# Optimization experiments

Measured on AMD Instinct MI355X. Metric: run time of the kernel, lower is better.

The kernel has to match this reference:

```python
import jax, jax.numpy as jnp
import numpy as np

# NOTE: the original source omits the definitions of QSVT, quantum_lcu_block,
# QuantumSumBlock and KANLayer. We reconstruct the standard math these blocks
# implement in quantum-KAN papers/repos:
#   QSVT(x)            -> vector of Chebyshev polynomials T_1..T_D of the
#                         (squashed) input, the polynomial basis QSVT realizes.
#   quantum_lcu_block  -> linear combination of unitaries: weighted sum of the
#                         QSVT vector normalized by the LCU l1 weight norm.
#   QuantumSumBlock    -> learnable interference sum: mean_k sin(alpha_k * v).
#   KANLayer           -> Chebyshev-KAN layer: spline term (Chebyshev basis
#                         contracted with coeffs) + SiLU base branch + bias.
# Everything is fully vectorized over (B, F) instead of the original per-scalar
# Python loops.

B, F, DEG, C, KBASIS = 16384, 512, 8, 10, 8


def _cheb(x, K):
    """Chebyshev features T_1..T_K of x in (-1, 1): shape x.shape + (K,)."""
    t = jnp.arccos(jnp.clip(x, -1.0, 1.0))
    k = jnp.arange(1, K + 1, dtype=x.dtype)
    return jnp.cos(t[..., None] * k)


def setup_inputs() -> dict:
    key = jax.random.key(0)
    ks = jax.random.split(key, 6)
    return {
        "X": jax.random.normal(ks[0], (B, F), dtype=jnp.float32),
        # nn.Parameter(torch.rand(num_features, degree))
        "lcu_weights": jax.random.uniform(ks[1], (F, DEG), dtype=jnp.float32),
        # one QuantumSumBlock(degree) per feature -> (F, DEG) phases
        "sum_alpha": jax.random.normal(ks[2], (F, DEG), dtype=jnp.float32),
        # KANLayer params
        "kan_coeff": jax.random.normal(ks[3], (C, F, KBASIS), dtype=jnp.float32) * 0.1,
        "kan_base": jax.random.normal(ks[4], (C, F), dtype=jnp.float32) * 0.1,
        "kan_bias": jnp.zeros((C,), dtype=jnp.float32),
    }


def reference(X, lcu_weights, sum_alpha, kan_coeff, kan_base, kan_bias):
    # squash inputs into the open interval (-1, 1) for the Chebyshev/QSVT basis
    x = 0.99 * jnp.tanh(X)                                   # (B, F)
    # QSVT polynomial feature vector per scalar, batched: (B, F, DEG)
    qsvt = _cheb(x, lcu_weights.shape[1])
    # LCU block: weighted combination normalized by l1 norm of weights -> (B, F)
    lcu = jnp.einsum('bfd,fd->bf', qsvt, lcu_weights) / (
        jnp.sum(jnp.abs(lcu_weights), axis=-1) + 1e-8)
    # Quantum sum block: learnable sinusoidal interference sum -> (B, F)
    summed = jnp.mean(jnp.sin(lcu[..., None] * sum_alpha), axis=-1)
    # Chebyshev-KAN layer
    s = 0.99 * jnp.tanh(summed)
    phi = _cheb(s, kan_coeff.shape[2])                       # (B, F, KBASIS)
    logits = (jnp.einsum('bfk,cfk->bc', phi, kan_coeff)
              + jax.nn.silu(summed) @ kan_base.T
              + kan_bias)                                    # (B, C)
    return logits
```

## Files before the change

kernel.cpp:

```cpp
#include <hip/hip_runtime.h>

#define BATCH 16384
#define NF    512
#define DEG   8
#define NC    10
#define KB    8

#define SPLITF 8
#define FC     (NF / SPLITF)
#define RB     64
#define PITCH  68
#define NT     256

#define CBN (NC * NF * KB)
#define BBN (NC * NF)
#define WS_PART (SPLITF * BATCH * NC)

#define INV2PI 0.15915494309189535f
#define LOG2E  1.4426950408889634f

typedef __attribute__((ext_vector_type(2))) float v2f;
typedef __attribute__((ext_vector_type(8))) short bfrag;
typedef __attribute__((ext_vector_type(4))) float f32x4;

union frag_u { bfrag s; unsigned u[4]; };

__device__ __forceinline__ v2f v2fma(v2f a, v2f b, v2f c) {
    return __builtin_elementwise_fma(a, b, c);
}
__device__ __forceinline__ v2f v2exp(v2f x) {
    v2f a = x * LOG2E;
    v2f r; r.x = __builtin_amdgcn_exp2f(a.x); r.y = __builtin_amdgcn_exp2f(a.y);
    return r;
}
__device__ __forceinline__ v2f v2rcp(v2f x) {
    v2f r; r.x = __builtin_amdgcn_rcpf(x.x); r.y = __builtin_amdgcn_rcpf(x.y);
    return r;
}
__device__ __forceinline__ v2f v2sin2pi(v2f x) {
    v2f r; r.x = __builtin_amdgcn_sinf(x.x); r.y = __builtin_amdgcn_sinf(x.y);
    return r;
}
__device__ __forceinline__ v2f v2tanh99(v2f x) {
    v2f e = v2exp(x + x);
    v2f r = v2rcp(e + 1.0f);
    return v2fma(r, (v2f)(-1.98f), (v2f)(0.99f));
}
__device__ __forceinline__ v2f v2silu(v2f v) {
    v2f e = v2exp(-v);
    v2f r = v2rcp(e + 1.0f);
    return v * r;
}
__device__ __forceinline__ unsigned bfpack2(float lo, float hi) {
    unsigned ul = __builtin_bit_cast(unsigned, lo) + 0x8000u;
    unsigned uh = __builtin_bit_cast(unsigned, hi) + 0x8000u;
    return __builtin_amdgcn_perm(uh, ul, 0x07060302);
}

__global__ __launch_bounds__(256) void prep_kernel(
    const float* __restrict__ coeff, const float* __restrict__ base,
    unsigned short* __restrict__ pk)
{
    const int i = blockIdx.x * 256 + threadIdx.x;
    if (i < CBN)
        pk[i] = (unsigned short)((__builtin_bit_cast(unsigned, coeff[i]) + 0x8000u) >> 16);
    else if (i < CBN + BBN)
        pk[i] = (unsigned short)((__builtin_bit_cast(unsigned, base[i - CBN]) + 0x8000u) >> 16);
}

__global__ __launch_bounds__(NT, 6) void qkan_kernel(
    const float* __restrict__ X,
    const float* __restrict__ lcu_w,
    const float* __restrict__ alpha,
    const unsigned short* __restrict__ pk,
    float* __restrict__ ws)
{
    __shared__ float s_mem[RB * PITCH];

    const int t      = threadIdx.x;
    const int rowblk = blockIdx.x >> 3;
    const int fsplit = blockIdx.x & (SPLITF - 1);
    const int row0   = rowblk * RB;
    const int fbase  = fsplit * FC;

    {
        const int f2   = t & 31;
        const int rsub = t >> 5;
        const int fA   = fbase + f2 * 2;

        float wa[2][DEG], aa[2][DEG], den[2];
#pragma unroll
        for (int i = 0; i < 2; ++i) {
            const float4 w0 = *(const float4*)(lcu_w + (fA + i) * DEG);
            const float4 w1 = *(const float4*)(lcu_w + (fA + i) * DEG + 4);
            const float4 a0 = *(const float4*)(alpha + (fA + i) * DEG);
            const float4 a1 = *(const float4*)(alpha + (fA + i) * DEG + 4);
            wa[i][0]=w0.x; wa[i][1]=w0.y; wa[i][2]=w0.z; wa[i][3]=w0.w;
            wa[i][4]=w1.x; wa[i][5]=w1.y; wa[i][6]=w1.z; wa[i][7]=w1.w;
            aa[i][0]=a0.x; aa[i][1]=a0.y; aa[i][2]=a0.z; aa[i][3]=a0.w;
            aa[i][4]=a1.x; aa[i][5]=a1.y; aa[i][6]=a1.z; aa[i][7]=a1.w;
            float d = 1e-8f;
#pragma unroll
            for (int k = 0; k < DEG; ++k) d += fabsf(wa[i][k]);
            den[i] = d;
        }
        v2f W[DEG], A2[DEG];
#pragma unroll
        for (int d = 0; d < DEG; ++d) {
            W[d]  = (v2f){wa[0][d], wa[1][d]};
            A2[d] = (v2f){aa[0][d] * INV2PI, aa[1][d] * INV2PI};
        }
        const v2f rden = (v2f){__builtin_amdgcn_rcpf(den[0]),
                               __builtin_amdgcn_rcpf(den[1])};

#pragma unroll
        for (int it = 0; it < RB / 8; ++it) {
            const int r = rsub + it * 8;
            const v2f xv = *(const v2f*)(X + (row0 + r) * NF + fA);
            const v2f x  = v2tanh99(xv);
            const v2f x2 = x + x;
            v2f tkm1 = (v2f){1.0f, 1.0f}, tk = x, num = (v2f){0.0f, 0.0f};
#pragma unroll
            for (int d = 0; d < DEG; ++d) {
                num = v2fma(W[d], tk, num);
                v2f tn = v2fma(x2, tk, -tkm1);
                tkm1 = tk; tk = tn;
            }
            const v2f lcu = num * rden;
            v2f ss = (v2f){0.0f, 0.0f};
#pragma unroll
            for (int d = 0; d < DEG; ++d)
                ss += v2sin2pi(lcu * A2[d]);
            *(v2f*)(&s_mem[r * PITCH + f2 * 2]) = ss * 0.125f;
        }
    }
    __syncthreads();

    const int lane = t & 63;
    const int wave = __builtin_amdgcn_readfirstlane(t >> 6);
    const int n    = lane & 15;
    const int q    = lane >> 4;
    const bool nv  = (n < NC);
    const int  ncl = nv ? n : (NC - 1);
    const int rl   = wave * 16 + n;

    const unsigned short* cb = pk;
    const unsigned short* bb = pk + CBN;
    const unsigned short* cbase = cb + (ncl * NF + fbase) * KB;

    f32x4 acc0 = {0.f, 0.f, 0.f, 0.f};
    f32x4 acc1 = {0.f, 0.f, 0.f, 0.f};

#pragma unroll 4
    for (int kp = 0; kp < 8; ++kp) {
        const bfrag b0 = *(const bfrag*)(cbase + (kp * 8 + q) * KB);
        const bfrag b1 = *(const bfrag*)(cbase + (kp * 8 + 4 + q) * KB);

        const float sA = s_mem[rl * PITCH + kp * 8 + q];
        const float sB = s_mem[rl * PITCH + kp * 8 + 4 + q];
        const v2f s  = v2tanh99((v2f){sA, sB});
        const v2f s2 = s + s;
        v2f T[KB];
        {
            v2f tkm1 = (v2f){1.0f, 1.0f}, tk = s;
#pragma unroll
            for (int k = 0; k < KB; ++k) {
                T[k] = tk;
                v2f tn = v2fma(s2, tk, -tkm1);
                tkm1 = tk; tk = tn;
            }
        }
        frag_u fa0, fa1;
#pragma unroll
        for (int i = 0; i < 4; ++i) {
            fa0.u[i] = bfpack2(T[2 * i].x, T[2 * i + 1].x);
            fa1.u[i] = bfpack2(T[2 * i].y, T[2 * i + 1].y);
        }
        acc0 = __builtin_amdgcn_mfma_f32_16x16x32_bf16(fa0.s, b0, acc0, 0, 0, 0);
        acc1 = __builtin_amdgcn_mfma_f32_16x16x32_bf16(fa1.s, b1, acc1, 0, 0, 0);
    }

#pragma unroll
    for (int kt2 = 0; kt2 < 2; ++kt2) {
        const bfrag b = *(const bfrag*)(bb + ncl * NF + fbase + kt2 * 32 + q * 8);
        const int off = kt2 * 32 + q * 8;
        const float4 v0 = *(const float4*)(&s_mem[rl * PITCH + off]);
        const float4 v1 = *(const float4*)(&s_mem[rl * PITCH + off + 4]);
        v2f vv[4] = {{v0.x, v0.y}, {v0.z, v0.w}, {v1.x, v1.y}, {v1.z, v1.w}};
        frag_u fa;
#pragma unroll
        for (int g = 0; g < 4; ++g) {
            const v2f sl = v2silu(vv[g]);
            fa.u[g] = bfpack2(sl.x, sl.y);
        }
        acc0 = __builtin_amdgcn_mfma_f32_16x16x32_bf16(fa.s, b, acc0, 0, 0, 0);
    }

    if (nv) {
        const f32x4 acc = acc0 + acc1;
        float* wsp = ws + (size_t)fsplit * (BATCH * NC);
#pragma unroll
        for (int i = 0; i < 4; ++i)
            wsp[(row0 + wave * 16 + q * 4 + i) * NC + n] = acc[i];
    }
}

__global__ __launch_bounds__(256) void reduce_kernel(
    const float* __restrict__ ws, const float* __restrict__ bias,
    float* __restrict__ out)
{
    const int idx = blockIdx.x * 256 + threadIdx.x;
    if (idx < BATCH * NC) {
        const int c = idx % NC;
        float v = bias[c];
#pragma unroll
        for (int s = 0; s < SPLITF; ++s)
            v += ws[(size_t)s * (BATCH * NC) + idx];
        out[idx] = v;
    }
}

extern "C" void kernel_launch(void* const* d_in, const int* in_sizes, int n_in,
                              void* d_out, int out_size, void* d_ws, size_t ws_size,
                              hipStream_t stream) {
    const float* X      = (const float*)d_in[0];
    const float* lcu_w  = (const float*)d_in[1];
    const float* alpha  = (const float*)d_in[2];
    const float* coeff  = (const float*)d_in[3];
    const float* base   = (const float*)d_in[4];
    const float* bias   = (const float*)d_in[5];
    float* out = (float*)d_out;
    float* ws  = (float*)d_ws;
    unsigned short* pk = (unsigned short*)(ws + WS_PART);

    prep_kernel<<<(CBN + BBN + 255) / 256, 256, 0, stream>>>(coeff, base, pk);
    qkan_kernel<<<(BATCH / RB) * SPLITF, NT, 0, stream>>>(X, lcu_w, alpha, pk, ws);
    reduce_kernel<<<(BATCH * NC + 255) / 256, 256, 0, stream>>>(ws, bias, out);
}
```

Before: 100.4 us.

## Fuse split-F reduction into main kernel via shared-memory cross-wave sum

Each block now handles 16 rows across all 512 features instead of 64 rows over one-eighth of the features. The four waves each cover a 128-feature slice and reduce their MFMA partial sums through shared memory, with the bias added in-kernel. This removes the global workspace write, the separate reduce kernel and its launch. It also switches bf16 packing to the round-to-nearest-even conversion intrinsic and lowers the occupancy hint, which may reduce latency hiding and reload the lcu and alpha weights in more blocks.

```diff
diff --git a/kernel.cpp b/kernel.cpp
--- a/kernel.cpp
+++ b/kernel.cpp
@@ -1,4 +1,5 @@
 #include <hip/hip_runtime.h>
+#include <hip/hip_bf16.h>
 
 #define BATCH 16384
 #define NF    512
@@ -6,15 +7,12 @@
 #define NC    10
 #define KB    8
 
-#define SPLITF 8
-#define FC     (NF / SPLITF)
-#define RB     64
-#define PITCH  68
-#define NT     256
+#define RB    16
+#define PITCH (NF + 4)
+#define NT    256
 
 #define CBN (NC * NF * KB)
 #define BBN (NC * NF)
-#define WS_PART (SPLITF * BATCH * NC)
 
 #define INV2PI 0.15915494309189535f
 #define LOG2E  1.4426950408889634f
@@ -51,10 +49,11 @@
     v2f r = v2rcp(e + 1.0f);
     return v * r;
 }
-__device__ __forceinline__ unsigned bfpack2(float lo, float hi) {
-    unsigned ul = __builtin_bit_cast(unsigned, lo) + 0x8000u;
-    unsigned uh = __builtin_bit_cast(unsigned, hi) + 0x8000u;
-    return __builtin_amdgcn_perm(uh, ul, 0x07060302);
+__device__ __forceinline__ unsigned cvtpk2(float lo, float hi) {
+    __hip_bfloat162 h = __float22bfloat162_rn(float2{lo, hi});
+    unsigned u;
+    __builtin_memcpy(&u, &h, sizeof(u));
+    return u;
 }
 
 __global__ __launch_bounds__(256) void prep_kernel(
@@ -68,25 +67,22 @@
         pk[i] = (unsigned short)((__builtin_bit_cast(unsigned, base[i - CBN]) + 0x8000u) >> 16);
 }
 
-__global__ __launch_bounds__(NT, 6) void qkan_kernel(
+__global__ __launch_bounds__(NT, 4) void qkan_kernel(
     const float* __restrict__ X,
     const float* __restrict__ lcu_w,
     const float* __restrict__ alpha,
     const unsigned short* __restrict__ pk,
-    float* __restrict__ ws)
+    const float* __restrict__ bias,
+    float* __restrict__ out)
 {
     __shared__ float s_mem[RB * PITCH];
-
-    const int t      = threadIdx.x;
-    const int rowblk = blockIdx.x >> 3;
-    const int fsplit = blockIdx.x & (SPLITF - 1);
-    const int row0   = rowblk * RB;
-    const int fbase  = fsplit * FC;
+    __shared__ float s_red[4 * RB * 16];
+
+    const int t    = threadIdx.x;
+    const int row0 = blockIdx.x * RB;
 
     {
-        const int f2   = t & 31;
-        const int rsub = t >> 5;
-        const int fA   = fbase + f2 * 2;
+        const int fA = t * 2;
 
         float wa[2][DEG], aa[2][DEG], den[2];
 #pragma unroll
@@ -113,9 +109,8 @@
         const v2f rden = (v2f){__builtin_amdgcn_rcpf(den[0]),
                                __builtin_amdgcn_rcpf(den[1])};
 
-#pragma unroll
-        for (int it = 0; it < RB / 8; ++it) {
-            const int r = rsub + it * 8;
+#pragma unroll 4
+        for (int r = 0; r < RB; ++r) {
             const v2f xv = *(const v2f*)(X + (row0 + r) * NF + fA);
             const v2f x  = v2tanh99(xv);
             const v2f x2 = x + x;
@@ -131,7 +126,7 @@
 #pragma unroll
             for (int d = 0; d < DEG; ++d)
                 ss += v2sin2pi(lcu * A2[d]);
-            *(v2f*)(&s_mem[r * PITCH + f2 * 2]) = ss * 0.125f;
+            *(v2f*)(&s_mem[r * PITCH + fA]) = ss * 0.125f;
         }
     }
     __syncthreads();
@@ -140,24 +135,23 @@
     const int wave = __builtin_amdgcn_readfirstlane(t >> 6);
     const int n    = lane & 15;
     const int q    = lane >> 4;
-    const bool nv  = (n < NC);
-    const int  ncl = nv ? n : (NC - 1);
-    const int rl   = wave * 16 + n;
+    const int ncl  = (n < NC) ? n : (NC - 1);
+    const int fw   = wave * 128;
 
     const unsigned short* cb = pk;
     const unsigned short* bb = pk + CBN;
-    const unsigned short* cbase = cb + (ncl * NF + fbase) * KB;
+    const unsigned short* cbase = cb + (ncl * NF + fw) * KB;
 
     f32x4 acc0 = {0.f, 0.f, 0.f, 0.f};
     f32x4 acc1 = {0.f, 0.f, 0.f, 0.f};
 
 #pragma unroll 4
-    for (int kp = 0; kp < 8; ++kp) {
+    for (int kp = 0; kp < 16; ++kp) {
         const bfrag b0 = *(const bfrag*)(cbase + (kp * 8 + q) * KB);
         const bfrag b1 = *(const bfrag*)(cbase + (kp * 8 + 4 + q) * KB);
 
-        const float sA = s_mem[rl * PITCH + kp * 8 + q];
-        const float sB = s_mem[rl * PITCH + kp * 8 + 4 + q];
+        const float sA = s_mem[n * PITCH + fw + kp * 8 + q];
+        const float sB = s_mem[n * PITCH + fw + kp * 8 + 4 + q];
         const v2f s  = v2tanh99((v2f){sA, sB});
         const v2f s2 = s + s;
         v2f T[KB];
@@ -173,50 +167,46 @@
         frag_u fa0, fa1;
 #pragma unroll
         for (int i = 0; i < 4; ++i) {
-            fa0.u[i] = bfpack2(T[2 * i].x, T[2 * i + 1].x);
-            fa1.u[i] = bfpack2(T[2 * i].y, T[2 * i + 1].y);
+            fa0.u[i] = cvtpk2(T[2 * i].x, T[2 * i + 1].x);
+            fa1.u[i] = cvtpk2(T[2 * i].y, T[2 * i + 1].y);
         }
         acc0 = __builtin_amdgcn_mfma_f32_16x16x32_bf16(fa0.s, b0, acc0, 0, 0, 0);
         acc1 = __builtin_amdgcn_mfma_f32_16x16x32_bf16(fa1.s, b1, acc1, 0, 0, 0);
     }
 
 #pragma unroll
-    for (int kt2 = 0; kt2 < 2; ++kt2) {
-        const bfrag b = *(const bfrag*)(bb + ncl * NF + fbase + kt2 * 32 + q * 8);
-        const int off = kt2 * 32 + q * 8;
-        const float4 v0 = *(const float4*)(&s_mem[rl * PITCH + off]);
-        const float4 v1 = *(const float4*)(&s_mem[rl * PITCH + off + 4]);
+    for (int kt2 = 0; kt2 < 4; ++kt2) {
+        const bfrag b = *(const bfrag*)(bb + ncl * NF + fw + kt2 * 32 + q * 8);
+        const int off = n * PITCH + fw + kt2 * 32 + q * 8;
+        const float4 v0 = *(const float4*)(&s_mem[off]);
+        const float4 v1 = *(const float4*)(&s_mem[off + 4]);
         v2f vv[4] = {{v0.x, v0.y}, {v0.z, v0.w}, {v1.x, v1.y}, {v1.z, v1.w}};
         frag_u fa;
 #pragma unroll
         for (int g = 0; g < 4; ++g) {
             const v2f sl = v2silu(vv[g]);
-            fa.u[g] = bfpack2(sl.x, sl.y);
-        }
-        acc0 = __builtin_amdgcn_mfma_f32_16x16x32_bf16(fa.s, b, acc0, 0, 0, 0);
-    }
-
-    if (nv) {
-        const f32x4 acc = acc0 + acc1;
-        float* wsp = ws + (size_t)fsplit * (BATCH * NC);
-#pragma unroll
-        for (int i = 0; i < 4; ++i)
-            wsp[(row0 + wave * 16 + q * 4 + i) * NC + n] = acc[i];
-    }
-}
-
-__global__ __launch_bounds__(256) void reduce_kernel(
-    const float* __restrict__ ws, const float* __restrict__ bias,
-    float* __restrict__ out)
-{
-    const int idx = blockIdx.x * 256 + threadIdx.x;
-    if (idx < BATCH * NC) {
-        const int c = idx % NC;
+            fa.u[g] = cvtpk2(sl.x, sl.y);
+        }
+        if (kt2 & 1)
+            acc1 = __builtin_amdgcn_mfma_f32_16x16x32_bf16(fa.s, b, acc1, 0, 0, 0);
+        else
+            acc0 = __builtin_amdgcn_mfma_f32_16x16x32_bf16(fa.s, b, acc0, 0, 0, 0);
+    }
+
+    const f32x4 acc = acc0 + acc1;
+#pragma unroll
+    for (int i = 0; i < 4; ++i)
+        s_red[(wave * RB + q * 4 + i) * 16 + n] = acc[i];
+    __syncthreads();
+
+    if (t < RB * NC) {
+        const int r = t / NC;
+        const int c = t - r * NC;
         float v = bias[c];
 #pragma unroll
-        for (int s = 0; s < SPLITF; ++s)
-            v += ws[(size_t)s * (BATCH * NC) + idx];
-        out[idx] = v;
+        for (int w = 0; w < 4; ++w)
+            v += s_red[(w * RB + r) * 16 + c];
+        out[(row0 + r) * NC + c] = v;
     }
 }
 
@@ -230,10 +220,8 @@
     const float* base   = (const float*)d_in[4];
     const float* bias   = (const float*)d_in[5];
     float* out = (float*)d_out;
-    float* ws  = (float*)d_ws;
-    unsigned short* pk = (unsigned short*)(ws + WS_PART);
+    unsigned short* pk = (unsigned short*)d_ws;
 
     prep_kernel<<<(CBN + BBN + 255) / 256, 256, 0, stream>>>(coeff, base, pk);
-    qkan_kernel<<<(BATCH / RB) * SPLITF, NT, 0, stream>>>(X, lcu_w, alpha, pk, ws);
-    reduce_kernel<<<(BATCH * NC + 255) / 256, 256, 0, stream>>>(ws, bias, out);
-}
+    qkan_kernel<<<BATCH / RB, NT, 0, stream>>>(X, lcu_w, alpha, pk, bias, out);
+}
```

Result: no change. 99.84 us (-0.5%).
